# Optimization experiments

Hardware: AMD Instinct MI355X
Metric: run time of the kernel (lower is better)

The kernel has to match this reference:

```python
import jax, jax.numpy as jnp
import numpy as np

EPS = 1e-8
C_RGLRU = 8.0  # Griffin constant

def rmsnorm(x, w):
    rms = jnp.sqrt(jnp.mean(x * x, axis=-1, keepdims=True) + EPS)
    return w * (x / rms)

def causal_depthwise_conv(x, conv_w, conv_b):
    # x: [B,S,H], conv_w: [K,H] depthwise causal conv, left-padded
    K = conv_w.shape[0]
    S = x.shape[1]
    xp = jnp.pad(x, ((0, 0), (K - 1, 0), (0, 0)))
    y = sum(conv_w[k] * xp[:, k:k + S, :] for k in range(K))
    return y + conv_b

def rg_lru(x, ga_W, ga_b, gx_W, gx_b, a_param):
    # x: [B,S,H]. Griffin RG-LRU: h_t = a_t h_{t-1} + sqrt(1-a_t^2) (i_t * x_t)
    r = jax.nn.sigmoid(x @ ga_W + ga_b)          # recurrence gate
    i = jax.nn.sigmoid(x @ gx_W + gx_b)          # input gate
    log_a = -C_RGLRU * jax.nn.softplus(a_param) * r
    a = jnp.exp(log_a)
    mult = jnp.sqrt(-jnp.expm1(2.0 * log_a))     # sqrt(1 - a^2), stable
    b = mult * (i * x)
    def combine(c1, c2):
        a1, b1 = c1
        a2, b2 = c2
        return a1 * a2, a2 * b1 + b2
    _, h = jax.lax.associative_scan(combine, (a, b), axis=1)
    return h

def setup_inputs() -> dict:
    D, H, F, K, B, S = 2048, 2048, 6144, 4, 2, 2048
    key = jax.random.key(0)
    ks = jax.random.split(key, 16)
    def lin(k, fan_in, shape):
        return jax.random.normal(k, shape, jnp.float32) * (fan_in ** -0.5)
    return {
        "x": jax.random.normal(ks[0], (B, S, D), jnp.float32),
        "norm1_w": jnp.ones((D,), jnp.float32),
        "left_W": lin(ks[1], D, (D, H)), "left_b": jnp.zeros((H,), jnp.float32),
        "right_W": lin(ks[2], D, (D, H)), "right_b": jnp.zeros((H,), jnp.float32),
        "conv_w": lin(ks[3], K, (K, H)), "conv_b": jnp.zeros((H,), jnp.float32),
        "ga_W": lin(ks[4], H, (H, H)), "ga_b": jnp.zeros((H,), jnp.float32),
        "gx_W": lin(ks[5], H, (H, H)), "gx_b": jnp.zeros((H,), jnp.float32),
        "a_param": jax.random.uniform(ks[6], (H,), jnp.float32, 0.5, 3.0),
        "out_W": lin(ks[7], H, (H, D)), "out_b": jnp.zeros((D,), jnp.float32),
        "norm2_w": jnp.ones((D,), jnp.float32),
        "up1_W": lin(ks[8], D, (D, F)), "up1_b": jnp.zeros((F,), jnp.float32),
        "up2_W": lin(ks[9], D, (D, F)), "up2_b": jnp.zeros((F,), jnp.float32),
        "down_W": lin(ks[10], F, (F, D)), "down_b": jnp.zeros((D,), jnp.float32),
    }

def reference(x, norm1_w, left_W, left_b, right_W, right_b, conv_w, conv_b,
              ga_W, ga_b, gx_W, gx_b, a_param, out_W, out_b,
              norm2_w, up1_W, up1_b, up2_W, up2_b, down_W, down_b):
    gelu = lambda t: jax.nn.gelu(t, approximate=False)
    # recurrent sub-block (pre-norm residual)
    xn = rmsnorm(x, norm1_w)
    left = gelu(xn @ left_W + left_b)
    right = rg_lru(causal_depthwise_conv(xn @ right_W + right_b, conv_w, conv_b),
                   ga_W, ga_b, gx_W, gx_b, a_param)
    x1 = (left * right) @ out_W + out_b + x
    # gated MLP sub-block (pre-norm residual)
    x1n = rmsnorm(x1, norm2_w)
    mlp = (gelu(x1n @ up1_W + up1_b) * (x1n @ up2_W + up2_b)) @ down_W + down_b
    return mlp + x1
```

## Files before the change

kernel.cpp:

```cpp
#include <hip/hip_runtime.h>
#include <cstdint>
#include <cstdio>

typedef __bf16 bf16x8 __attribute__((ext_vector_type(8)));
typedef float  f32x4  __attribute__((ext_vector_type(4)));
typedef const __attribute__((address_space(1))) void* gas_ptr;
typedef __attribute__((address_space(3))) void* las_ptr;

__device__ __forceinline__ uint16_t f32_to_bf16_rne(float f){
  uint32_t u = __builtin_bit_cast(uint32_t, f);
  u += 0x7FFFu + ((u >> 16) & 1u);
  return (uint16_t)(u >> 16);
}
__device__ __forceinline__ float bf16_to_f32(uint16_t h){
  uint32_t u = (uint32_t)h << 16;
  return __builtin_bit_cast(float, u);
}
__device__ __forceinline__ float gelu_exact(float x){
  return 0.5f * x * (1.f + erff(x * 0.7071067811865475f));
}

template<int EPI, int BM>
__global__ __launch_bounds__(512)
void gemm2p(const uint16_t* __restrict__ A, const uint16_t* __restrict__ Bt,
            const float* __restrict__ bias0, const float* __restrict__ bias1,
            const float* __restrict__ auxF, const uint16_t* __restrict__ auxB,
            float* __restrict__ Cf, uint16_t* __restrict__ Cb0, uint16_t* __restrict__ Cb1,
            int M, int N, int K, int SPLIT)
{
  constexpr int BN = 256;
  constexpr int M_REP   = BM / 32;
  constexpr int LOADS_A = BM / 64;
  constexpr int LOADS_B = BN / 64;
  constexpr int ABYTES  = 2 * BM * 128;
  __shared__ alignas(16) char smem[2 * (BM + BN) * 128];

  const int tid  = threadIdx.x;
  const int lane = tid & 63;
  const int wid  = tid >> 6;
  const int wm = wid >> 2, wn = wid & 3;
  const int la = lane & 15, lq = lane >> 4;
  const int n0 = blockIdx.x * BN;
  const int m0 = blockIdx.y * BM;

  const int rt = tid >> 3;
  const int gs = (tid & 7) ^ (rt & 7);
  const uint16_t* srcA = A  + (size_t)(m0 + rt) * K + gs * 8;
  const uint16_t* srcB = Bt + (size_t)(n0 + rt) * K + gs * 8;

  const int rowAb = (wm * (BM / 2) + la) * 128;
  const int rowBb = (wn * 64 + la) * 128;
  const int ck0 = ((lq)     ^ (la & 7)) * 16;
  const int ck1 = ((4 + lq) ^ (la & 7)) * 16;

  f32x4 acc[M_REP][4];
  const f32x4 fz = {0.f, 0.f, 0.f, 0.f};
#pragma unroll
  for (int m = 0; m < M_REP; ++m)
#pragma unroll
    for (int n = 0; n < 4; ++n) acc[m][n] = fz;

  const int NT = K >> 6;

#define STAGE(KT, BUF) do {                                                   \
    const uint16_t* sa_ = srcA + (size_t)(KT) * 64;                           \
    const uint16_t* sb_ = srcB + (size_t)(KT) * 64;                           \
    _Pragma("unroll")                                                         \
    for (int l = 0; l < LOADS_A; ++l)                                         \
      __builtin_amdgcn_global_load_lds((gas_ptr)(sa_ + (size_t)l * 64 * K),   \
          (las_ptr)(smem + (BUF) * BM * 128 + (l * 512 + tid) * 16), 16, 0, 0);\
    _Pragma("unroll")                                                         \
    for (int l = 0; l < LOADS_B; ++l)                                         \
      __builtin_amdgcn_global_load_lds((gas_ptr)(sb_ + (size_t)l * 64 * K),   \
          (las_ptr)(smem + ABYTES + (BUF) * BN * 128 + (l * 512 + tid) * 16), \
          16, 0, 0);                                                          \
  } while (0)

  STAGE(0, 0);
  asm volatile("s_waitcnt vmcnt(0)" ::: "memory");
  __builtin_amdgcn_s_barrier();

  int cur = 0;
  for (int kt = 0; kt < NT; ++kt) {
    const bool pf = (kt + 1 < NT);
    if (pf) STAGE(kt + 1, cur ^ 1);

    const char* bufA = smem + cur * BM * 128;
    const char* bufB = smem + ABYTES + cur * BN * 128;

    bf16x8 bF[4][2];
#pragma unroll
    for (int n = 0; n < 4; ++n) {
      int ro = (int)(bufB - smem) + rowBb + n * 2048;
      bF[n][0] = *(const bf16x8*)(smem + ro + ck0);
      bF[n][1] = *(const bf16x8*)(smem + ro + ck1);
    }
    __builtin_amdgcn_s_setprio(1);
#pragma unroll
    for (int m = 0; m < M_REP; ++m) {
      int ro = (int)(bufA - smem) + rowAb + m * 2048;
      bf16x8 a0 = *(const bf16x8*)(smem + ro + ck0);
      bf16x8 a1 = *(const bf16x8*)(smem + ro + ck1);
#pragma unroll
      for (int n = 0; n < 4; ++n) {
        acc[m][n] = __builtin_amdgcn_mfma_f32_16x16x32_bf16(a0, bF[n][0], acc[m][n], 0, 0, 0);
        acc[m][n] = __builtin_amdgcn_mfma_f32_16x16x32_bf16(a1, bF[n][1], acc[m][n], 0, 0, 0);
      }
    }
    __builtin_amdgcn_s_setprio(0);

    if (pf) {
      asm volatile("s_waitcnt vmcnt(0)" ::: "memory");
      __builtin_amdgcn_s_barrier();
      cur ^= 1;
    }
  }
#undef STAGE

#pragma unroll
  for (int n = 0; n < 4; ++n) {
    int col = n0 + wn * 64 + n * 16 + la;
    const bool second = (col >= SPLIT);
    float bv = second ? bias1[col - SPLIT] : bias0[col];
#pragma unroll
    for (int m = 0; m < M_REP; ++m) {
      int rbase = m0 + wm * (BM / 2) + m * 16 + lq * 4;
#pragma unroll
      for (int r = 0; r < 4; ++r) {
        int row = rbase + r;
        size_t idx = (size_t)row * N + col;
        float v = acc[m][n][r] + bv;
        if constexpr (EPI == 0) Cf[idx] = v + auxF[idx];
        if constexpr (EPI == 1) {
          if (!second) Cb0[(size_t)row * SPLIT + col] = f32_to_bf16_rne(gelu_exact(v));
          else         Cb1[(size_t)row * (N - SPLIT) + (col - SPLIT)] = f32_to_bf16_rne(v);
        }
        if constexpr (EPI == 2) Cb0[idx] = f32_to_bf16_rne(v);
        if constexpr (EPI == 3) Cb0[idx] = f32_to_bf16_rne(v * bf16_to_f32(auxB[idx]));
      }
    }
  }
}

__global__ __launch_bounds__(256)
void cvt_transpose(const float* __restrict__ in, uint16_t* __restrict__ out, int R, int C)
{
  __shared__ float tile[64][65];
  const int r0 = blockIdx.y * 64, c0 = blockIdx.x * 64;
  const int t = threadIdx.x;
  const int lc = (t & 15) * 4;
  const int lr0 = t >> 4;
#pragma unroll
  for (int j = 0; j < 4; j++){
    int lr = lr0 + j*16;
    float4 v = *(const float4*)(in + (size_t)(r0 + lr) * C + c0 + lc);
    tile[lr][lc+0] = v.x; tile[lr][lc+1] = v.y; tile[lr][lc+2] = v.z; tile[lr][lc+3] = v.w;
  }
  __syncthreads();
  const int oc = t >> 2;
  const int rseg = (t & 3) * 16;
  alignas(16) uint16_t tmp[16];
#pragma unroll
  for (int j = 0; j < 16; j++) tmp[j] = f32_to_bf16_rne(tile[rseg + j][oc]);
  uint4* dst = (uint4*)(out + (size_t)(c0 + oc) * R + r0 + rseg);
  dst[0] = *(const uint4*)(&tmp[0]);
  dst[1] = *(const uint4*)(&tmp[8]);
}

__global__ __launch_bounds__(256)
void rmsnorm_kernel(const float* __restrict__ x, const float* __restrict__ w,
                    uint16_t* __restrict__ out, int D)
{
  const int row = blockIdx.x;
  const float* xr = x + (size_t)row * D;
  const int base = threadIdx.x * 8;
  float4 va = *(const float4*)(xr + base);
  float4 vb = *(const float4*)(xr + base + 4);
  float ss = va.x*va.x + va.y*va.y + va.z*va.z + va.w*va.w
           + vb.x*vb.x + vb.y*vb.y + vb.z*vb.z + vb.w*vb.w;
#pragma unroll
  for (int o = 32; o > 0; o >>= 1) ss += __shfl_xor(ss, o);
  __shared__ float red[4];
  if ((threadIdx.x & 63) == 0) red[threadIdx.x >> 6] = ss;
  __syncthreads();
  float tot = red[0] + red[1] + red[2] + red[3];
  float inv = rsqrtf(tot / (float)D + 1e-8f);
  float4 wa = *(const float4*)(w + base);
  float4 wb = *(const float4*)(w + base + 4);
  alignas(16) uint16_t tmp[8];
  tmp[0] = f32_to_bf16_rne(va.x * wa.x * inv);
  tmp[1] = f32_to_bf16_rne(va.y * wa.y * inv);
  tmp[2] = f32_to_bf16_rne(va.z * wa.z * inv);
  tmp[3] = f32_to_bf16_rne(va.w * wa.w * inv);
  tmp[4] = f32_to_bf16_rne(vb.x * wb.x * inv);
  tmp[5] = f32_to_bf16_rne(vb.y * wb.y * inv);
  tmp[6] = f32_to_bf16_rne(vb.z * wb.z * inv);
  tmp[7] = f32_to_bf16_rne(vb.w * wb.w * inv);
  *(uint4*)(out + (size_t)row * D + base) = *(const uint4*)tmp;
}

__global__ __launch_bounds__(256)
void conv_kernel(const uint16_t* __restrict__ xin, const float* __restrict__ cw,
                 const float* __restrict__ cb, uint16_t* __restrict__ yout,
                 int S, int H)
{
  const int h = blockIdx.x * 256 + threadIdx.x;
  const int b = blockIdx.z;
  const int t0 = blockIdx.y * 128;
  const float w0 = cw[h], w1 = cw[H + h], w2 = cw[2*H + h], w3 = cw[3*H + h];
  const float bias = cb[h];
  const size_t colbase = (size_t)b * S * H + h;
  float xm3 = (t0 >= 3) ? bf16_to_f32(xin[colbase + (size_t)(t0-3)*H]) : 0.f;
  float xm2 = (t0 >= 2) ? bf16_to_f32(xin[colbase + (size_t)(t0-2)*H]) : 0.f;
  float xm1 = (t0 >= 1) ? bf16_to_f32(xin[colbase + (size_t)(t0-1)*H]) : 0.f;
  for (int t = t0; t < t0 + 128; ++t){
    size_t idx = colbase + (size_t)t * H;
    float xt = bf16_to_f32(xin[idx]);
    float y = w0*xm3 + w1*xm2 + w2*xm1 + w3*xt + bias;
    yout[idx] = f32_to_bf16_rne(y);
    xm3 = xm2; xm2 = xm1; xm1 = xt;
  }
}

__device__ __forceinline__ void rglru_ab(float rp, float ip, float xc, float coef,
                                         float& a, float& bb)
{
  float r  = 1.f / (1.f + expf(-rp));
  float la = coef * r;
  a = expf(la);
  float mult = sqrtf(-expm1f(2.f * la));
  float ig = 1.f / (1.f + expf(-ip));
  bb = mult * ig * xc;
}

__global__ __launch_bounds__(256)
void scan_phase1(const uint16_t* __restrict__ gpre, const uint16_t* __restrict__ convb,
                 const float* __restrict__ ap,
                 float* __restrict__ SA, float* __restrict__ SB,
                 int S, int H, int T0, int NC)
{
  const int h = blockIdx.x * 256 + threadIdx.x;
  const int j = blockIdx.y, b = blockIdx.z;
  const float coef = -8.f * log1pf(expf(ap[h]));
  size_t rowb = (size_t)b * S + (size_t)j * T0;
  float A = 1.f, Bc = 0.f;
  for (int t = 0; t < T0; ++t){
    size_t row = rowb + t;
    float rp = bf16_to_f32(gpre[row * 2 * H + h]);
    float ip = bf16_to_f32(gpre[row * 2 * H + H + h]);
    float xc = bf16_to_f32(convb[row * H + h]);
    float a, bb; rglru_ab(rp, ip, xc, coef, a, bb);
    A *= a; Bc = a * Bc + bb;
  }
  size_t o = ((size_t)b * NC + j) * H + h;
  SA[o] = A; SB[o] = Bc;
}

__global__ __launch_bounds__(256)
void scan_phase2(const float* __restrict__ SA, const float* __restrict__ SB,
                 float* __restrict__ SH, int H, int NC)
{
  const int h = blockIdx.x * 256 + threadIdx.x;
  const int b = blockIdx.y;
  float hh = 0.f;
  for (int j = 0; j < NC; ++j){
    size_t o = ((size_t)b * NC + j) * H + h;
    SH[o] = hh;
    hh = SA[o] * hh + SB[o];
  }
}

__global__ __launch_bounds__(256)
void scan_phase3(const uint16_t* __restrict__ gpre, const uint16_t* __restrict__ convb,
                 const float* __restrict__ ap, const float* __restrict__ SH,
                 const uint16_t* __restrict__ left, uint16_t* __restrict__ lr,
                 int S, int H, int T0, int NC)
{
  const int h = blockIdx.x * 256 + threadIdx.x;
  const int j = blockIdx.y, b = blockIdx.z;
  const float coef = -8.f * log1pf(expf(ap[h]));
  float hh = SH[((size_t)b * NC + j) * H + h];
  size_t rowb = (size_t)b * S + (size_t)j * T0;
  for (int t = 0; t < T0; ++t){
    size_t row = rowb + t;
    float rp = bf16_to_f32(gpre[row * 2 * H + h]);
    float ip = bf16_to_f32(gpre[row * 2 * H + H + h]);
    float xc = bf16_to_f32(convb[row * H + h]);
    float a, bb; rglru_ab(rp, ip, xc, coef, a, bb);
    hh = a * hh + bb;
    lr[row * H + h] = f32_to_bf16_rne(bf16_to_f32(left[row * H + h]) * hh);
  }
}

extern "C" void kernel_launch(void* const* d_in, const int* in_sizes, int n_in,
                              void* d_out, int out_size, void* d_ws, size_t ws_size,
                              hipStream_t stream)
{
  const int B = 2, S = 2048, D = 2048, H = 2048, F = 6144;
  const int M = B * S;
  const int NC = 32, T0 = S / NC;

  const float* x       = (const float*)d_in[0];
  const float* norm1_w = (const float*)d_in[1];
  const float* left_W  = (const float*)d_in[2];
  const float* left_b  = (const float*)d_in[3];
  const float* right_W = (const float*)d_in[4];
  const float* right_b = (const float*)d_in[5];
  const float* conv_w  = (const float*)d_in[6];
  const float* conv_b  = (const float*)d_in[7];
  const float* ga_W    = (const float*)d_in[8];
  const float* ga_b    = (const float*)d_in[9];
  const float* gx_W    = (const float*)d_in[10];
  const float* gx_b    = (const float*)d_in[11];
  const float* a_param = (const float*)d_in[12];
  const float* out_W   = (const float*)d_in[13];
  const float* out_b   = (const float*)d_in[14];
  const float* norm2_w = (const float*)d_in[15];
  const float* up1_W   = (const float*)d_in[16];
  const float* up1_b   = (const float*)d_in[17];
  const float* up2_W   = (const float*)d_in[18];
  const float* up2_b   = (const float*)d_in[19];
  const float* down_W  = (const float*)d_in[20];
  const float* down_b  = (const float*)d_in[21];

  char* ws = (char*)d_ws;
  size_t off = 0;
  auto alloc = [&](size_t bytes) -> char* {
    char* p = ws + off; off += (bytes + 255) & ~(size_t)255; return p;
  };
  uint16_t* WT    = (uint16_t*)alloc((size_t)F * D * 2);
  uint16_t* XN    = (uint16_t*)alloc((size_t)M * D * 2);
  uint16_t* LEFT  = (uint16_t*)alloc((size_t)M * H * 2);
  uint16_t* RPRE  = (uint16_t*)alloc((size_t)M * H * 2);
  uint16_t* CONVB = (uint16_t*)alloc((size_t)M * H * 2);
  uint16_t* GPRE  = (uint16_t*)alloc((size_t)M * 2 * H * 2);
  uint16_t* LR    = (uint16_t*)alloc((size_t)M * H * 2);
  float*    X1    = (float*)   alloc((size_t)M * D * 4);
  uint16_t* X1N   = (uint16_t*)alloc((size_t)M * D * 2);
  float*    SA    = (float*)   alloc((size_t)B * NC * H * 4);
  float*    SB    = (float*)   alloc((size_t)B * NC * H * 4);
  float*    SHB   = (float*)   alloc((size_t)B * NC * H * 4);
  uint16_t* T1    = XN;
  uint16_t* G     = CONVB;

  if (off > ws_size) {
    fprintf(stderr, "kernel_launch: ws too small, need %zu have %zu\n", off, ws_size);
    return;
  }

  float* OUT = (float*)d_out;
  dim3 blk(256);
  dim3 gblk(512);

  rmsnorm_kernel<<<M, blk, 0, stream>>>(x, norm1_w, XN, D);

  cvt_transpose<<<dim3(H/64, D/64), blk, 0, stream>>>(left_W, WT, D, H);
  cvt_transpose<<<dim3(H/64, D/64), blk, 0, stream>>>(right_W, WT + (size_t)H * D, D, H);
  gemm2p<1, 256><<<dim3((2*H)/256, M/256), gblk, 0, stream>>>(
      XN, WT, left_b, right_b, nullptr, nullptr, nullptr, LEFT, RPRE, M, 2*H, D, H);

  conv_kernel<<<dim3(H/256, S/128, B), blk, 0, stream>>>(RPRE, conv_w, conv_b, CONVB, S, H);

  cvt_transpose<<<dim3(H/64, H/64), blk, 0, stream>>>(ga_W, WT, H, H);
  cvt_transpose<<<dim3(H/64, H/64), blk, 0, stream>>>(gx_W, WT + (size_t)H * H, H, H);
  gemm2p<2, 256><<<dim3((2*H)/256, M/256), gblk, 0, stream>>>(
      CONVB, WT, ga_b, gx_b, nullptr, nullptr, nullptr, GPRE, nullptr, M, 2*H, H, H);

  scan_phase1<<<dim3(H/256, NC, B), blk, 0, stream>>>(GPRE, CONVB, a_param, SA, SB, S, H, T0, NC);
  scan_phase2<<<dim3(H/256, B), blk, 0, stream>>>(SA, SB, SHB, H, NC);
  scan_phase3<<<dim3(H/256, NC, B), blk, 0, stream>>>(GPRE, CONVB, a_param, SHB, LEFT, LR, S, H, T0, NC);

  cvt_transpose<<<dim3(D/64, H/64), blk, 0, stream>>>(out_W, WT, H, D);
  gemm2p<0, 128><<<dim3(D/256, M/128), gblk, 0, stream>>>(
      LR, WT, out_b, out_b, x, nullptr, X1, nullptr, nullptr, M, D, H, D);

  rmsnorm_kernel<<<M, blk, 0, stream>>>(X1, norm2_w, X1N, D);

  cvt_transpose<<<dim3(F/64, D/64), blk, 0, stream>>>(up1_W, WT, D, F);
  gemm2p<1, 256><<<dim3(F/256, M/256), gblk, 0, stream>>>(
      X1N, WT, up1_b, up1_b, nullptr, nullptr, nullptr, T1, nullptr, M, F, D, F);

  cvt_transpose<<<dim3(F/64, D/64), blk, 0, stream>>>(up2_W, WT, D, F);
  gemm2p<3, 256><<<dim3(F/256, M/256), gblk, 0, stream>>>(
      X1N, WT, up2_b, up2_b, nullptr, T1, nullptr, G, nullptr, M, F, D, F);

  cvt_transpose<<<dim3(D/64, F/64), blk, 0, stream>>>(down_W, WT, F, D);
  gemm2p<0, 128><<<dim3(D/256, M/128), gblk, 0, stream>>>(
      G, WT, down_b, down_b, X1, nullptr, OUT, nullptr, nullptr, M, D, F, D);
}
```

Measured before the change: 819.3 us.

## Add 8-phase 256x256 GEMM, fuse up1/up2 projections, store residual in bf16

Adds a new GEMM kernel (gemm8p) with a 256x256 tile. It keeps two K-tiles in flight and splits each K-step into four MFMA phases separated by barriers, interleaving LDS reads and global prefetch. The left/right, gate and now-concatenated up1/up2 projections use it, replacing two separate MLP up GEMMs plus an aux-multiply epilogue with one wide GEMM and a separate elementwise multiply kernel. The intermediate residual X1 is stored in bf16 instead of fp32, with a bf16 rmsnorm variant, which cuts memory traffic at some cost in precision of the residual path.

Result: faster. 782.8 us (-4.5%).

```diff
diff --git a/kernel.cpp b/kernel.cpp
--- a/kernel.cpp
+++ b/kernel.cpp
@@ -18,6 +18,145 @@
 }
 __device__ __forceinline__ float gelu_exact(float x){
   return 0.5f * x * (1.f + erff(x * 0.7071067811865475f));
+}
+
+template<int EPI>
+__device__ __forceinline__ void epi_store(float v, size_t idx, int row, int col,
+    int N, int SPLIT, const float* auxF, const uint16_t* auxB,
+    float* Cf, uint16_t* Cb0, uint16_t* Cb1, bool second)
+{
+  if constexpr (EPI == 1) {
+    if (!second) Cb0[(size_t)row * SPLIT + col] = f32_to_bf16_rne(gelu_exact(v));
+    else         Cb1[(size_t)row * (N - SPLIT) + (col - SPLIT)] = f32_to_bf16_rne(v);
+  }
+  if constexpr (EPI == 2) Cb0[idx] = f32_to_bf16_rne(v);
+  if constexpr (EPI == 4) Cb0[idx] = f32_to_bf16_rne(v + auxF[idx]);
+  if constexpr (EPI == 5) Cf[idx] = v + bf16_to_f32(auxB[idx]);
+}
+
+template<int EPI>
+__global__ __launch_bounds__(512)
+void gemm8p(const uint16_t* __restrict__ A, const uint16_t* __restrict__ Bt,
+            const float* __restrict__ bias0, const float* __restrict__ bias1,
+            const float* __restrict__ auxF, const uint16_t* __restrict__ auxB,
+            float* __restrict__ Cf, uint16_t* __restrict__ Cb0, uint16_t* __restrict__ Cb1,
+            int M, int N, int K, int SPLIT)
+{
+  __shared__ alignas(16) char smem[131072];
+  const int tid = threadIdx.x, lane = tid & 63, wid = tid >> 6;
+  const int wm = wid >> 2, wn = wid & 3;
+  const int la = lane & 15, lq = lane >> 4;
+  const int n0 = blockIdx.x * 256, m0 = blockIdx.y * 256;
+
+  const int rt = tid >> 3;
+  const int gs = (tid & 7) ^ (rt & 7);
+  const uint16_t* srcA = A  + (size_t)(m0 + rt) * K + gs * 8;
+  const uint16_t* srcB = Bt + (size_t)(n0 + rt) * K + gs * 8;
+
+  const int rowAb = (wm * 128 + la) * 128;
+  const int rowBb = (wn * 64 + la) * 128;
+  const int ck0 = ((lq)     ^ (la & 7)) * 16;
+  const int ck1 = ((4 + lq) ^ (la & 7)) * 16;
+
+  f32x4 acc[8][4];
+  const f32x4 fz = {0.f, 0.f, 0.f, 0.f};
+#pragma unroll
+  for (int m = 0; m < 8; ++m)
+#pragma unroll
+    for (int n = 0; n < 4; ++n) acc[m][n] = fz;
+
+  bf16x8 aF[4][2], bF0[2][2], bF1[2][2];
+  const int NT = K >> 6;
+
+#define STAGE_A8(KT, BUF) do { _Pragma("unroll")                              \
+    for (int l = 0; l < 4; ++l)                                               \
+      __builtin_amdgcn_global_load_lds(                                       \
+          (gas_ptr)(srcA + (size_t)(KT) * 64 + (size_t)l * 64 * K),           \
+          (las_ptr)(smem + (BUF) * 32768 + (l * 512 + tid) * 16), 16, 0, 0);  \
+  } while (0)
+#define STAGE_B8(KT, BUF) do { _Pragma("unroll")                              \
+    for (int l = 0; l < 4; ++l)                                               \
+      __builtin_amdgcn_global_load_lds(                                       \
+          (gas_ptr)(srcB + (size_t)(KT) * 64 + (size_t)l * 64 * K),           \
+          (las_ptr)(smem + 65536 + (BUF) * 32768 + (l * 512 + tid) * 16),     \
+          16, 0, 0);                                                          \
+  } while (0)
+#define RD_B8(DST, NH, BUF) do { _Pragma("unroll")                            \
+    for (int nq = 0; nq < 2; ++nq) {                                          \
+      int ro_ = 65536 + (BUF) * 32768 + rowBb + ((NH) * 2 + nq) * 2048;       \
+      DST[nq][0] = *(const bf16x8*)(smem + ro_ + ck0);                        \
+      DST[nq][1] = *(const bf16x8*)(smem + ro_ + ck1);                        \
+    }                                                                         \
+  } while (0)
+#define RD_A8(MHS, BUF) do { _Pragma("unroll")                                \
+    for (int mq = 0; mq < 4; ++mq) {                                          \
+      int ro_ = (BUF) * 32768 + rowAb + ((MHS) * 4 + mq) * 2048;              \
+      aF[mq][0] = *(const bf16x8*)(smem + ro_ + ck0);                         \
+      aF[mq][1] = *(const bf16x8*)(smem + ro_ + ck1);                         \
+    }                                                                         \
+  } while (0)
+#define MM8(MHS, NH, BF) do { _Pragma("unroll")                               \
+    for (int mq = 0; mq < 4; ++mq)                                            \
+      _Pragma("unroll")                                                       \
+      for (int nq = 0; nq < 2; ++nq) {                                        \
+        acc[(MHS)*4+mq][(NH)*2+nq] = __builtin_amdgcn_mfma_f32_16x16x32_bf16( \
+            aF[mq][0], BF[nq][0], acc[(MHS)*4+mq][(NH)*2+nq], 0, 0, 0);       \
+        acc[(MHS)*4+mq][(NH)*2+nq] = __builtin_amdgcn_mfma_f32_16x16x32_bf16( \
+            aF[mq][1], BF[nq][1], acc[(MHS)*4+mq][(NH)*2+nq], 0, 0, 0);       \
+      }                                                                       \
+  } while (0)
+#define BARR() __builtin_amdgcn_s_barrier()
+
+  STAGE_A8(0, 0); STAGE_B8(0, 0);
+  STAGE_A8(1, 1); STAGE_B8(1, 1);
+  asm volatile("s_waitcnt vmcnt(8)" ::: "memory");
+  BARR();
+
+  for (int t = 0; t < NT; ++t) {
+    const int buf = t & 1;
+    const bool pf = (t + 2 < NT);
+    RD_B8(bF0, 0, buf); RD_A8(0, buf);
+    BARR();
+    __builtin_amdgcn_s_setprio(1); MM8(0, 0, bF0); __builtin_amdgcn_s_setprio(0);
+    BARR();
+    RD_B8(bF1, 1, buf);
+    BARR();
+    __builtin_amdgcn_s_setprio(1); MM8(0, 1, bF1); __builtin_amdgcn_s_setprio(0);
+    BARR();
+    RD_A8(1, buf);
+    if (pf) STAGE_B8(t + 2, buf);
+    BARR();
+    __builtin_amdgcn_s_setprio(1); MM8(1, 0, bF0); __builtin_amdgcn_s_setprio(0);
+    BARR();
+    if (pf) STAGE_A8(t + 2, buf);
+    BARR();
+    __builtin_amdgcn_s_setprio(1); MM8(1, 1, bF1); __builtin_amdgcn_s_setprio(0);
+    asm volatile("s_waitcnt vmcnt(8)" ::: "memory");
+    BARR();
+  }
+#undef STAGE_A8
+#undef STAGE_B8
+#undef RD_B8
+#undef RD_A8
+#undef MM8
+#undef BARR
+
+#pragma unroll
+  for (int n = 0; n < 4; ++n) {
+    int col = n0 + wn * 64 + n * 16 + la;
+    const bool second = (col >= SPLIT);
+    float bv = second ? bias1[col - SPLIT] : bias0[col];
+#pragma unroll
+    for (int m = 0; m < 8; ++m) {
+      int rbase = m0 + wm * 128 + m * 16 + lq * 4;
+#pragma unroll
+      for (int r = 0; r < 4; ++r) {
+        int row = rbase + r;
+        size_t idx = (size_t)row * N + col;
+        epi_store<EPI>(acc[m][n][r] + bv, idx, row, col, N, SPLIT, auxF, auxB, Cf, Cb0, Cb1, second);
+      }
+    }
+  }
 }
 
 template<int EPI, int BM>
@@ -85,20 +224,20 @@
     const bool pf = (kt + 1 < NT);
     if (pf) STAGE(kt + 1, cur ^ 1);
 
-    const char* bufA = smem + cur * BM * 128;
-    const char* bufB = smem + ABYTES + cur * BN * 128;
+    const int offA = cur * BM * 128;
+    const int offB = ABYTES + cur * BN * 128;
 
     bf16x8 bF[4][2];
 #pragma unroll
     for (int n = 0; n < 4; ++n) {
-      int ro = (int)(bufB - smem) + rowBb + n * 2048;
+      int ro = offB + rowBb + n * 2048;
       bF[n][0] = *(const bf16x8*)(smem + ro + ck0);
       bF[n][1] = *(const bf16x8*)(smem + ro + ck1);
     }
     __builtin_amdgcn_s_setprio(1);
 #pragma unroll
     for (int m = 0; m < M_REP; ++m) {
-      int ro = (int)(bufA - smem) + rowAb + m * 2048;
+      int ro = offA + rowAb + m * 2048;
       bf16x8 a0 = *(const bf16x8*)(smem + ro + ck0);
       bf16x8 a1 = *(const bf16x8*)(smem + ro + ck1);
 #pragma unroll
@@ -129,14 +268,7 @@
       for (int r = 0; r < 4; ++r) {
         int row = rbase + r;
         size_t idx = (size_t)row * N + col;
-        float v = acc[m][n][r] + bv;
-        if constexpr (EPI == 0) Cf[idx] = v + auxF[idx];
-        if constexpr (EPI == 1) {
-          if (!second) Cb0[(size_t)row * SPLIT + col] = f32_to_bf16_rne(gelu_exact(v));
-          else         Cb1[(size_t)row * (N - SPLIT) + (col - SPLIT)] = f32_to_bf16_rne(v);
-        }
-        if constexpr (EPI == 2) Cb0[idx] = f32_to_bf16_rne(v);
-        if constexpr (EPI == 3) Cb0[idx] = f32_to_bf16_rne(v * bf16_to_f32(auxB[idx]));
+        epi_store<EPI>(acc[m][n][r] + bv, idx, row, col, N, SPLIT, auxF, auxB, Cf, Cb0, Cb1, second);
       }
     }
   }
@@ -197,6 +329,50 @@
   tmp[6] = f32_to_bf16_rne(vb.z * wb.z * inv);
   tmp[7] = f32_to_bf16_rne(vb.w * wb.w * inv);
   *(uint4*)(out + (size_t)row * D + base) = *(const uint4*)tmp;
+}
+
+__global__ __launch_bounds__(256)
+void rmsnorm_bf16_kernel(const uint16_t* __restrict__ x, const float* __restrict__ w,
+                         uint16_t* __restrict__ out, int D)
+{
+  const int row = blockIdx.x;
+  const uint16_t* xr = x + (size_t)row * D;
+  const int base = threadIdx.x * 8;
+  uint4 v = *(const uint4*)(xr + base);
+  const uint16_t* vp = (const uint16_t*)&v;
+  float xs[8];
+  float ss = 0.f;
+#pragma unroll
+  for (int j = 0; j < 8; ++j){ xs[j] = bf16_to_f32(vp[j]); ss += xs[j]*xs[j]; }
+#pragma unroll
+  for (int o = 32; o > 0; o >>= 1) ss += __shfl_xor(ss, o);
+  __shared__ float red[4];
+  if ((threadIdx.x & 63) == 0) red[threadIdx.x >> 6] = ss;
+  __syncthreads();
+  float tot = red[0] + red[1] + red[2] + red[3];
+  float inv = rsqrtf(tot / (float)D + 1e-8f);
+  float4 wa = *(const float4*)(w + base);
+  float4 wb = *(const float4*)(w + base + 4);
+  float wv[8] = {wa.x, wa.y, wa.z, wa.w, wb.x, wb.y, wb.z, wb.w};
+  alignas(16) uint16_t tmp[8];
+#pragma unroll
+  for (int j = 0; j < 8; ++j) tmp[j] = f32_to_bf16_rne(xs[j] * wv[j] * inv);
+  *(uint4*)(out + (size_t)row * D + base) = *(const uint4*)tmp;
+}
+
+__global__ __launch_bounds__(256)
+void mul_kernel(uint16_t* __restrict__ t1, const uint16_t* __restrict__ u2)
+{
+  size_t i = ((size_t)blockIdx.x * 256 + threadIdx.x) * 8;
+  uint4 a = *(const uint4*)(t1 + i);
+  uint4 b = *(const uint4*)(u2 + i);
+  const uint16_t* ap = (const uint16_t*)&a;
+  const uint16_t* bp = (const uint16_t*)&b;
+  alignas(16) uint16_t o[8];
+#pragma unroll
+  for (int j = 0; j < 8; ++j)
+    o[j] = f32_to_bf16_rne(bf16_to_f32(ap[j]) * bf16_to_f32(bp[j]));
+  *(uint4*)(t1 + i) = *(const uint4*)o;
 }
 
 __global__ __launch_bounds__(256)
@@ -328,20 +504,20 @@
   auto alloc = [&](size_t bytes) -> char* {
     char* p = ws + off; off += (bytes + 255) & ~(size_t)255; return p;
   };
-  uint16_t* WT    = (uint16_t*)alloc((size_t)F * D * 2);
+  uint16_t* WT    = (uint16_t*)alloc((size_t)2 * F * D * 2);
   uint16_t* XN    = (uint16_t*)alloc((size_t)M * D * 2);
   uint16_t* LEFT  = (uint16_t*)alloc((size_t)M * H * 2);
   uint16_t* RPRE  = (uint16_t*)alloc((size_t)M * H * 2);
   uint16_t* CONVB = (uint16_t*)alloc((size_t)M * H * 2);
   uint16_t* GPRE  = (uint16_t*)alloc((size_t)M * 2 * H * 2);
   uint16_t* LR    = (uint16_t*)alloc((size_t)M * H * 2);
-  float*    X1    = (float*)   alloc((size_t)M * D * 4);
+  uint16_t* X1B   = (uint16_t*)alloc((size_t)M * D * 2);
   uint16_t* X1N   = (uint16_t*)alloc((size_t)M * D * 2);
   float*    SA    = (float*)   alloc((size_t)B * NC * H * 4);
   float*    SB    = (float*)   alloc((size_t)B * NC * H * 4);
   float*    SHB   = (float*)   alloc((size_t)B * NC * H * 4);
   uint16_t* T1    = XN;
-  uint16_t* G     = CONVB;
+  uint16_t* U2    = CONVB;
 
   if (off > ws_size) {
     fprintf(stderr, "kernel_launch: ws too small, need %zu have %zu\n", off, ws_size);
@@ -356,14 +532,14 @@
 
   cvt_transpose<<<dim3(H/64, D/64), blk, 0, stream>>>(left_W, WT, D, H);
   cvt_transpose<<<dim3(H/64, D/64), blk, 0, stream>>>(right_W, WT + (size_t)H * D, D, H);
-  gemm2p<1, 256><<<dim3((2*H)/256, M/256), gblk, 0, stream>>>(
+  gemm8p<1><<<dim3((2*H)/256, M/256), gblk, 0, stream>>>(
       XN, WT, left_b, right_b, nullptr, nullptr, nullptr, LEFT, RPRE, M, 2*H, D, H);
 
   conv_kernel<<<dim3(H/256, S/128, B), blk, 0, stream>>>(RPRE, conv_w, conv_b, CONVB, S, H);
 
   cvt_transpose<<<dim3(H/64, H/64), blk, 0, stream>>>(ga_W, WT, H, H);
   cvt_transpose<<<dim3(H/64, H/64), blk, 0, stream>>>(gx_W, WT + (size_t)H * H, H, H);
-  gemm2p<2, 256><<<dim3((2*H)/256, M/256), gblk, 0, stream>>>(
+  gemm8p<2><<<dim3((2*H)/256, M/256), gblk, 0, stream>>>(
       CONVB, WT, ga_b, gx_b, nullptr, nullptr, nullptr, GPRE, nullptr, M, 2*H, H, H);
 
   scan_phase1<<<dim3(H/256, NC, B), blk, 0, stream>>>(GPRE, CONVB, a_param, SA, SB, S, H, T0, NC);
@@ -371,20 +547,19 @@
   scan_phase3<<<dim3(H/256, NC, B), blk, 0, stream>>>(GPRE, CONVB, a_param, SHB, LEFT, LR, S, H, T0, NC);
 
   cvt_transpose<<<dim3(D/64, H/64), blk, 0, stream>>>(out_W, WT, H, D);
-  gemm2p<0, 128><<<dim3(D/256, M/128), gblk, 0, stream>>>(
-      LR, WT, out_b, out_b, x, nullptr, X1, nullptr, nullptr, M, D, H, D);
-
-  rmsnorm_kernel<<<M, blk, 0, stream>>>(X1, norm2_w, X1N, D);
+  gemm2p<4, 128><<<dim3(D/256, M/128), gblk, 0, stream>>>(
+      LR, WT, out_b, out_b, x, nullptr, nullptr, X1B, nullptr, M, D, H, D);
+
+  rmsnorm_bf16_kernel<<<M, blk, 0, stream>>>(X1B, norm2_w, X1N, D);
 
   cvt_transpose<<<dim3(F/64, D/64), blk, 0, stream>>>(up1_W, WT, D, F);
-  gemm2p<1, 256><<<dim3(F/256, M/256), gblk, 0, stream>>>(
-      X1N, WT, up1_b, up1_b, nullptr, nullptr, nullptr, T1, nullptr, M, F, D, F);
-
-  cvt_transpose<<<dim3(F/64, D/64), blk, 0, stream>>>(up2_W, WT, D, F);
-  gemm2p<3, 256><<<dim3(F/256, M/256), gblk, 0, stream>>>(
-      X1N, WT, up2_b, up2_b, nullptr, T1, nullptr, G, nullptr, M, F, D, F);
+  cvt_transpose<<<dim3(F/64, D/64), blk, 0, stream>>>(up2_W, WT + (size_t)F * D, D, F);
+  gemm8p<1><<<dim3((2*F)/256, M/256), gblk, 0, stream>>>(
+      X1N, WT, up1_b, up2_b, nullptr, nullptr, nullptr, T1, U2, M, 2*F, D, F);
+
+  mul_kernel<<<dim3((unsigned)((size_t)M * F / 8 / 256)), blk, 0, stream>>>(T1, U2);
 
   cvt_transpose<<<dim3(D/64, F/64), blk, 0, stream>>>(down_W, WT, F, D);
-  gemm2p<0, 128><<<dim3(D/256, M/128), gblk, 0, stream>>>(
-      G, WT, down_b, down_b, X1, nullptr, OUT, nullptr, nullptr, M, D, F, D);
-}
+  gemm2p<5, 128><<<dim3(D/256, M/128), gblk, 0, stream>>>(
+      T1, WT, down_b, down_b, nullptr, X1B, OUT, nullptr, nullptr, M, D, F, D);
+}
```
